# Kernel tuning notes

Hardware: AMD Instinct MI355X
Metric: run time of the kernel (lower is better)

The kernel has to match this reference:

```python
import jax, jax.numpy as jnp
import numpy as np

NUM_HEADS = 8
LN_EPS = 1e-5


def _layernorm(t, w, b):
    mu = t.mean(-1, keepdims=True)
    var = t.var(-1, keepdims=True)  # ddof=0, matches torch LayerNorm
    return (t - mu) * jax.lax.rsqrt(var + LN_EPS) * w + b


def setup_inputs() -> dict:
    key = jax.random.key(0)
    ks = jax.random.split(key, 5)
    B, C, H, W = 16, 384, 32, 32
    hidden = 4 * C
    s = 0.02
    return {
        "x": jax.random.normal(ks[0], (B, C, H, W), jnp.float32),
        "ln1_w": jnp.ones((C,), jnp.float32),
        "ln1_b": jnp.zeros((C,), jnp.float32),
        "qkv_w": s * jax.random.normal(ks[1], (3 * C, C), jnp.float32),
        "qkv_b": jnp.zeros((3 * C,), jnp.float32),
        "proj_w": s * jax.random.normal(ks[2], (C, C), jnp.float32),
        "proj_b": jnp.zeros((C,), jnp.float32),
        "ln2_w": jnp.ones((C,), jnp.float32),
        "ln2_b": jnp.zeros((C,), jnp.float32),
        "fc1_w": s * jax.random.normal(ks[3], (hidden, C), jnp.float32),
        "fc1_b": jnp.zeros((hidden,), jnp.float32),
        "fc2_w": s * jax.random.normal(ks[4], (C, hidden), jnp.float32),
        "fc2_b": jnp.zeros((C,), jnp.float32),
    }


def reference(x, ln1_w, ln1_b, qkv_w, qkv_b, proj_w, proj_b,
              ln2_w, ln2_b, fc1_w, fc1_b, fc2_w, fc2_b):
    B, C, H, W = x.shape
    N = H * W
    nh = NUM_HEADS
    hd = C // nh
    scale = hd ** (-0.5)

    xf = x.reshape(B, C, N).transpose(0, 2, 1)  # (B, N, C) tokens

    # --- pre-norm attention ---
    h1 = _layernorm(xf, ln1_w, ln1_b)
    qkv = h1 @ qkv_w.T + qkv_b                      # (B, N, 3C)
    qkv = qkv.reshape(B, N, 3, nh, hd).transpose(2, 0, 3, 1, 4)  # (3,B,h,N,d)
    q, k, v = qkv[0], qkv[1], qkv[2]
    attn = jax.nn.softmax(jnp.einsum('bhnd,bhmd->bhnm', q, k) * scale, axis=-1)
    out = jnp.einsum('bhnm,bhmd->bhnd', attn, v)    # (B,h,N,d)
    out = out.transpose(0, 2, 1, 3).reshape(B, N, C)
    out = out @ proj_w.T + proj_b
    xf = xf + out

    # --- pre-norm FFN (exact GELU, matching torch nn.GELU default) ---
    h2 = _layernorm(xf, ln2_w, ln2_b)
    f = jax.nn.gelu(h2 @ fc1_w.T + fc1_b, approximate=False)
    f = f @ fc2_w.T + fc2_b
    xf = xf + f

    return xf.transpose(0, 2, 1).reshape(B, C, H, W)
```

## Files before the change

### kernel.cpp

```cpp
#include <hip/hip_runtime.h>

typedef unsigned short u16;
using bf16x8 = __attribute__((ext_vector_type(8))) short;
using f32x4  = __attribute__((ext_vector_type(4))) float;

#define DEV __device__ __forceinline__

constexpr int    NTOK = 16384;
constexpr size_t QKSZ = (size_t)16 * 8 * 1024 * 64;
constexpr float  ATTN_SCALE = 0.14433756729740645f;

DEV u16 f2bf(float x) {
  unsigned int u = __float_as_uint(x);
  u += 0x7fffu + ((u >> 16) & 1u);
  return (u16)(u >> 16);
}

DEV void async16(const u16* g, u16* l) {
  __builtin_amdgcn_global_load_lds(
      (const __attribute__((address_space(1))) unsigned int*)g,
      (__attribute__((address_space(3))) unsigned int*)l, 16, 0, 0);
}

DEV const bf16x8* lds_swz(const u16* base, int row, int bytecol) {
  int byte = row * 128 + bytecol;
  byte ^= (row & 7) << 4;
  return (const bf16x8*)((const char*)base + byte);
}

DEV float gelu_f(float x) { return 0.5f * x * (1.0f + erff(x * 0.70710678118654752440f)); }

__global__ void cvt4_kernel(const float* __restrict__ s0, u16* __restrict__ d0,
                            const float* __restrict__ s1, u16* __restrict__ d1,
                            const float* __restrict__ s2, u16* __restrict__ d2,
                            const float* __restrict__ s3, u16* __restrict__ d3) {
  int i = blockIdx.x * 256 + threadIdx.x;
  const float* s; u16* d; int off;
  if (i < 110592)        { s = s0; d = d0; off = i; }
  else if (i < 147456)   { s = s1; d = d1; off = i - 110592; }
  else if (i < 294912)   { s = s2; d = d2; off = i - 147456; }
  else                   { s = s3; d = d3; off = i - 294912; }
  float4 v = *(const float4*)(s + (size_t)off * 4);
  ushort4 o{f2bf(v.x), f2bf(v.y), f2bf(v.z), f2bf(v.w)};
  *(ushort4*)(d + (size_t)off * 4) = o;
}

__global__ __launch_bounds__(256) void ln_kernel(
    const float* __restrict__ in, const float* __restrict__ gw,
    const float* __restrict__ gb, u16* __restrict__ out) {
  __shared__ float tile[32][385];
  __shared__ float mu_s[32], rs_s[32];
  const int b = blockIdx.y;
  const int n0 = blockIdx.x * 32;
  const int t = threadIdx.x;
  const int j = t & 31, cb = t >> 5;
  const float* src = in + (size_t)b * 384 * 1024 + n0;
  for (int k = 0; k < 48; ++k) {
    int c = k * 8 + cb;
    tile[j][c] = src[(size_t)c * 1024 + j];
  }
  __syncthreads();
  const int jt = t >> 3, r = t & 7;
  float s = 0.f, ss = 0.f;
  for (int c = r; c < 384; c += 8) { float v = tile[jt][c]; s += v; ss += v * v; }
  s += __shfl_xor(s, 1); ss += __shfl_xor(ss, 1);
  s += __shfl_xor(s, 2); ss += __shfl_xor(ss, 2);
  s += __shfl_xor(s, 4); ss += __shfl_xor(ss, 4);
  const float mean = s * (1.f / 384.f);
  const float var  = ss * (1.f / 384.f) - mean * mean;
  if (r == 0) { mu_s[jt] = mean; rs_s[jt] = rsqrtf(var + 1e-5f); }
  __syncthreads();
  for (int q = t; q < 3072; q += 256) {
    int tok = q / 96, c4 = (q - tok * 96) * 4;
    float m = mu_s[tok], rv = rs_s[tok];
    float4 wv = *(const float4*)(gw + c4);
    float4 bv = *(const float4*)(gb + c4);
    u16* dst = out + (size_t)(b * 1024 + n0 + tok) * 384 + c4;
    ushort4 o{f2bf((tile[tok][c4 + 0] - m) * rv * wv.x + bv.x),
              f2bf((tile[tok][c4 + 1] - m) * rv * wv.y + bv.y),
              f2bf((tile[tok][c4 + 2] - m) * rv * wv.z + bv.z),
              f2bf((tile[tok][c4 + 3] - m) * rv * wv.w + bv.w)};
    *(ushort4*)dst = o;
  }
}

template<int EPI>
__global__ __launch_bounds__(256, 2) void gemm_kernel(
    const u16* __restrict__ A, const u16* __restrict__ W,
    const float* __restrict__ bias, float* __restrict__ outf,
    u16* __restrict__ outh, const float* __restrict__ resid, int K) {
  __shared__ u16 sA[2][4096], sB[2][4096];
  const int m0 = blockIdx.x * 128, n0 = blockIdx.y * 128;
  const int wv = threadIdx.x >> 6, lane = threadIdx.x & 63;
  const int wm = (wv >> 1) * 64, wn = (wv & 1) * 64;
  const int l16 = lane & 15, lg8 = (lane >> 4) * 8;

  f32x4 acc[4][4];
#pragma unroll
  for (int i = 0; i < 4; ++i)
#pragma unroll
    for (int jj = 0; jj < 4; ++jj) acc[i][jj] = f32x4{0.f, 0.f, 0.f, 0.f};

  const int nk = K >> 5;
  auto stage = [&](int buf, int kt) {
    const u16* Ab = A + (size_t)m0 * K + kt * 32;
    const u16* Wb = W + (size_t)n0 * K + kt * 32;
#pragma unroll
    for (int i = 0; i < 2; ++i) {
      int chunk = i * 256 + wv * 64 + lane;
      int row = chunk >> 2, sl = chunk & 3;
      async16(Ab + (size_t)row * K + sl * 8, &sA[buf][(i * 256 + wv * 64) * 8]);
      async16(Wb + (size_t)row * K + sl * 8, &sB[buf][(i * 256 + wv * 64) * 8]);
    }
  };
  stage(0, 0);
  __syncthreads();
  int cur = 0;
  for (int kt = 0; kt < nk; ++kt) {
    if (kt + 1 < nk) stage(cur ^ 1, kt + 1);
    bf16x8 av[4], bv[4];
#pragma unroll
    for (int f = 0; f < 4; ++f) {
      av[f] = *(const bf16x8*)&sA[cur][(wm + f * 16 + l16) * 32 + lg8];
      bv[f] = *(const bf16x8*)&sB[cur][(wn + f * 16 + l16) * 32 + lg8];
    }
#pragma unroll
    for (int mf = 0; mf < 4; ++mf)
#pragma unroll
      for (int nf = 0; nf < 4; ++nf)
        acc[mf][nf] = __builtin_amdgcn_mfma_f32_16x16x32_bf16(av[mf], bv[nf], acc[mf][nf], 0, 0, 0);
    __syncthreads();
    cur ^= 1;
  }

#pragma unroll
  for (int mf = 0; mf < 4; ++mf) {
    const int mm = m0 + wm + mf * 16 + (lane >> 4) * 4;
    const int b = mm >> 10, nn = mm & 1023;
#pragma unroll
    for (int nf = 0; nf < 4; ++nf) {
      const int col = n0 + wn + nf * 16 + l16;
      f32x4 v = acc[mf][nf];
      const float bs = bias[col];
      if constexpr (EPI == 0) {
        const int which = col / 384, rem = col % 384;
        const int hh = rem / 48, dd = rem % 48;
        if (which == 2) {
          unsigned long long pk = 0;
#pragma unroll
          for (int rr = 0; rr < 4; ++rr)
            pk |= (unsigned long long)f2bf(v[rr] + bs) << (16 * rr);
          size_t idx = 2ull * QKSZ + (((size_t)((b * 8 + hh) * 64 + dd)) << 10) + nn;
          *(unsigned long long*)&outh[idx] = pk;
        } else {
          const float sc = (which == 0) ? ATTN_SCALE : 1.0f;
          size_t base = (size_t)which * QKSZ + (size_t)((b * 8 + hh) * 1024 + nn) * 64 + dd;
#pragma unroll
          for (int rr = 0; rr < 4; ++rr) outh[base + (size_t)rr * 64] = f2bf((v[rr] + bs) * sc);
        }
      } else if constexpr (EPI == 1 || EPI == 3) {
        size_t idx = ((size_t)(b * 384 + col) << 10) + nn;
        float4 rr4 = *(const float4*)&resid[idx];
        float4 o{v[0] + bs + rr4.x, v[1] + bs + rr4.y, v[2] + bs + rr4.z, v[3] + bs + rr4.w};
        *(float4*)&outf[idx] = o;
      } else {
#pragma unroll
        for (int rr = 0; rr < 4; ++rr)
          outh[(size_t)(mm + rr) * 1536 + col] = f2bf(gelu_f(v[rr] + bs));
      }
    }
  }
}

__global__ __launch_bounds__(256, 2) void attn_kernel(
    const u16* __restrict__ Qg, const u16* __restrict__ Kg,
    const u16* __restrict__ Vtg, u16* __restrict__ outp) {
  __shared__ u16 Ks[2][64 * 64];
  __shared__ u16 Vs[2][64 * 64];
  __shared__ u16 QPs[4 * 32 * 72];
  const int orig = blockIdx.x;
  const int swz = (orig & 7) * 128 + (orig >> 3);
  const int bh = swz >> 3, qt = swz & 7;
  const int w = threadIdx.x >> 6, lane = threadIdx.x & 63;
  const int l16 = lane & 15, lg = lane >> 4;

  const u16* kbase = Kg + (size_t)bh * 1024 * 64;
  const u16* vbase = Vtg + (size_t)bh * 64 * 1024;

  auto stageKV = [&](int buf, int kv) {
#pragma unroll
    for (int i = 0; i < 2; ++i) {
      int cb = (i * 4 + w) * 64;
      int ck = cb + lane;
      int g  = ck ^ ((ck >> 3) & 7);
      async16(kbase + (size_t)kv * 4096 + g * 8, &Ks[buf][cb * 8]);
      async16(vbase + (size_t)(g >> 3) * 1024 + kv * 64 + (g & 7) * 8, &Vs[buf][cb * 8]);
    }
  };

  {
    const u16* src = Qg + (size_t)(bh * 1024 + qt * 128) * 64;
#pragma unroll
    for (int i = 0; i < 4; ++i) {
      int cb = (i * 4 + w) * 64;
      int ck = cb + lane;
      int g  = ck ^ ((ck >> 3) & 7);
      async16(src + g * 8, &QPs[cb * 8]);
    }
  }
  stageKV(0, 0);
  __syncthreads();

  bf16x8 qf[2][2];
#pragma unroll
  for (int mf = 0; mf < 2; ++mf)
#pragma unroll
    for (int ks = 0; ks < 2; ++ks)
      qf[mf][ks] = *lds_swz(QPs, w * 32 + mf * 16 + l16, ks * 64 + lg * 16);
  __syncthreads();

  float lr[2][4];
  f32x4 acco[2][4];
#pragma unroll
  for (int mf = 0; mf < 2; ++mf) {
#pragma unroll
    for (int r = 0; r < 4; ++r) lr[mf][r] = 0.f;
#pragma unroll
    for (int df = 0; df < 4; ++df) acco[mf][df] = f32x4{0.f, 0.f, 0.f, 0.f};
  }
  u16* Pw = &QPs[w * 32 * 72];

  int cur = 0;
  for (int kv = 0; kv < 16; ++kv) {
    if (kv + 1 < 16) stageKV(cur ^ 1, kv + 1);

    f32x4 accs[2][4];
#pragma unroll
    for (int mf = 0; mf < 2; ++mf)
#pragma unroll
      for (int nf = 0; nf < 4; ++nf) accs[mf][nf] = f32x4{0.f, 0.f, 0.f, 0.f};
    __builtin_amdgcn_s_setprio(1);
#pragma unroll
    for (int nf = 0; nf < 4; ++nf) {
      bf16x8 k0 = *lds_swz(Ks[cur], nf * 16 + l16, lg * 16);
      bf16x8 k1 = *lds_swz(Ks[cur], nf * 16 + l16, 64 + lg * 16);
#pragma unroll
      for (int mf = 0; mf < 2; ++mf) {
        accs[mf][nf] = __builtin_amdgcn_mfma_f32_16x16x32_bf16(qf[mf][0], k0, accs[mf][nf], 0, 0, 0);
        accs[mf][nf] = __builtin_amdgcn_mfma_f32_16x16x32_bf16(qf[mf][1], k1, accs[mf][nf], 0, 0, 0);
      }
    }
    __builtin_amdgcn_s_setprio(0);
#pragma unroll
    for (int mf = 0; mf < 2; ++mf)
#pragma unroll
      for (int r = 0; r < 4; ++r) {
        float s0 = __expf(accs[mf][0][r]);
        float s1 = __expf(accs[mf][1][r]);
        float s2 = __expf(accs[mf][2][r]);
        float s3 = __expf(accs[mf][3][r]);
        accs[mf][0][r] = s0; accs[mf][1][r] = s1;
        accs[mf][2][r] = s2; accs[mf][3][r] = s3;
        lr[mf][r] += s0 + s1 + s2 + s3;
      }
#pragma unroll
    for (int mf = 0; mf < 2; ++mf)
#pragma unroll
      for (int nf = 0; nf < 4; ++nf)
#pragma unroll
        for (int r = 0; r < 4; ++r)
          Pw[(mf * 16 + lg * 4 + r) * 72 + nf * 16 + l16] = f2bf(accs[mf][nf][r]);
    asm volatile("s_waitcnt lgkmcnt(0)" ::: "memory");
#pragma unroll
    for (int ks = 0; ks < 2; ++ks) {
      bf16x8 pa[2], vf[4];
#pragma unroll
      for (int mf = 0; mf < 2; ++mf)
        pa[mf] = *(const bf16x8*)&Pw[(mf * 16 + l16) * 72 + ks * 32 + lg * 8];
#pragma unroll
      for (int df = 0; df < 4; ++df)
        vf[df] = *lds_swz(Vs[cur], df * 16 + l16, ks * 64 + lg * 16);
      __builtin_amdgcn_s_setprio(1);
#pragma unroll
      for (int mf = 0; mf < 2; ++mf)
#pragma unroll
        for (int df = 0; df < 4; ++df)
          acco[mf][df] = __builtin_amdgcn_mfma_f32_16x16x32_bf16(pa[mf], vf[df], acco[mf][df], 0, 0, 0);
      __builtin_amdgcn_s_setprio(0);
    }
    __syncthreads();
    cur ^= 1;
  }
  const int b = bh >> 3, h = bh & 7;
#pragma unroll
  for (int mf = 0; mf < 2; ++mf)
#pragma unroll
    for (int r = 0; r < 4; ++r) {
      float t = lr[mf][r];
      t += __shfl_xor(t, 1); t += __shfl_xor(t, 2);
      t += __shfl_xor(t, 4); t += __shfl_xor(t, 8);
      float inv = 1.f / t;
      int token = qt * 128 + w * 32 + mf * 16 + lg * 4 + r;
      size_t rowb = (size_t)(b * 1024 + token) * 384 + h * 48;
#pragma unroll
      for (int df = 0; df < 3; ++df)
        outp[rowb + df * 16 + l16] = f2bf(acco[mf][df][r] * inv);
    }
}

constexpr size_t OFF_WQKV = 0;
constexpr size_t OFF_WPROJ = 884736;
constexpr size_t OFF_WFC1 = 1179648;
constexpr size_t OFF_WFC2 = 2359296;
constexpr size_t OFF_H    = 3538944;
constexpr size_t OFF_QKV  = 16121856;
constexpr size_t OFF_AO   = 66453504;
constexpr size_t OFF_Y1T  = 79036416;

extern "C" void kernel_launch(void* const* d_in, const int* in_sizes, int n_in,
                              void* d_out, int out_size, void* d_ws, size_t ws_size,
                              hipStream_t stream) {
  (void)in_sizes; (void)n_in; (void)out_size; (void)ws_size;
  const float* x     = (const float*)d_in[0];
  const float* ln1w  = (const float*)d_in[1];
  const float* ln1b  = (const float*)d_in[2];
  const float* qkvw  = (const float*)d_in[3];
  const float* qkvbi = (const float*)d_in[4];
  const float* projw = (const float*)d_in[5];
  const float* projb = (const float*)d_in[6];
  const float* ln2w  = (const float*)d_in[7];
  const float* ln2b  = (const float*)d_in[8];
  const float* fc1w  = (const float*)d_in[9];
  const float* fc1b  = (const float*)d_in[10];
  const float* fc2w  = (const float*)d_in[11];
  const float* fc2b  = (const float*)d_in[12];

  char* ws = (char*)d_ws;
  u16* wqkv  = (u16*)(ws + OFF_WQKV);
  u16* wproj = (u16*)(ws + OFF_WPROJ);
  u16* wfc1  = (u16*)(ws + OFF_WFC1);
  u16* wfc2  = (u16*)(ws + OFF_WFC2);
  u16* h1    = (u16*)(ws + OFF_H);
  u16* qkvs  = (u16*)(ws + OFF_QKV);
  u16* f1    = qkvs;
  u16* ao    = (u16*)(ws + OFF_AO);
  float* y1t = (float*)(ws + OFF_Y1T);

  hipMemsetAsync(qkvs, 0, QKSZ * 2, stream);

  cvt4_kernel<<<1728, 256, 0, stream>>>(qkvw, wqkv, projw, wproj, fc1w, wfc1, fc2w, wfc2);

  dim3 lngrid(32, 16);
  ln_kernel<<<lngrid, 256, 0, stream>>>(x, ln1w, ln1b, h1);

  gemm_kernel<0><<<dim3(NTOK / 128, 9), 256, 0, stream>>>(h1, wqkv, qkvbi, nullptr, qkvs, nullptr, 384);

  attn_kernel<<<dim3(1024), 256, 0, stream>>>(qkvs, qkvs + QKSZ, qkvs + 2 * QKSZ, ao);

  gemm_kernel<1><<<dim3(NTOK / 128, 3), 256, 0, stream>>>(ao, wproj, projb, y1t, nullptr, x, 384);

  ln_kernel<<<lngrid, 256, 0, stream>>>(y1t, ln2w, ln2b, h1 );

  gemm_kernel<2><<<dim3(NTOK / 128, 12), 256, 0, stream>>>(h1, wfc1, fc1b, nullptr, f1, nullptr, 384);

  gemm_kernel<3><<<dim3(NTOK / 128, 3), 256, 0, stream>>>(f1, wfc2, fc2b, (float*)d_out, nullptr, y1t, 1536);
}
```

Measured before the change: 308.0 us.

## Triple-buffer GEMM/attention loads, pad QKV weights, swap MFMA operands, tanh GELU

GEMM and attention K/V staging move from double to triple buffering, with explicit vmcnt waits and a single barrier per iteration, and the GEMM gains an XOR-swizzled LDS layout. QKV weights and bias are padded to 64 per head with the attention scale folded in, which removes the memset and allows vectorized Q/K stores. The V part of QKV gets its own transposed-store GEMM variant, and the fc1/QKV GEMMs swap MFMA operands so they can write packed 8-byte stores. Exact erf GELU is replaced by the tanh approximation, which changes numerics relative to the exact-GELU reference.

```diff
diff --git a/kernel.cpp b/kernel.cpp
--- a/kernel.cpp
+++ b/kernel.cpp
@@ -28,21 +28,48 @@
   return (const bf16x8*)((const char*)base + byte);
 }
 
-DEV float gelu_f(float x) { return 0.5f * x * (1.0f + erff(x * 0.70710678118654752440f)); }
-
-__global__ void cvt4_kernel(const float* __restrict__ s0, u16* __restrict__ d0,
-                            const float* __restrict__ s1, u16* __restrict__ d1,
-                            const float* __restrict__ s2, u16* __restrict__ d2,
-                            const float* __restrict__ s3, u16* __restrict__ d3) {
+DEV float gelu_f(float x) {
+  float y = 0.7978845608028654f * (x + 0.044715f * x * x * x);
+  float e = __expf(2.f * y);
+  float t = 1.f - 2.f / (e + 1.f);
+  return 0.5f * x * (1.f + t);
+}
+
+__global__ void cvt_kernel(const float* __restrict__ qkvw, const float* __restrict__ qkvb,
+                           const float* __restrict__ projw, const float* __restrict__ fc1w,
+                           const float* __restrict__ fc2w,
+                           u16* __restrict__ wqkvp, float* __restrict__ biasp,
+                           u16* __restrict__ wproj, u16* __restrict__ wfc1,
+                           u16* __restrict__ wfc2) {
   int i = blockIdx.x * 256 + threadIdx.x;
-  const float* s; u16* d; int off;
-  if (i < 110592)        { s = s0; d = d0; off = i; }
-  else if (i < 147456)   { s = s1; d = d1; off = i - 110592; }
-  else if (i < 294912)   { s = s2; d = d2; off = i - 147456; }
-  else                   { s = s3; d = d3; off = i - 294912; }
-  float4 v = *(const float4*)(s + (size_t)off * 4);
-  ushort4 o{f2bf(v.x), f2bf(v.y), f2bf(v.z), f2bf(v.w)};
-  *(ushort4*)(d + (size_t)off * 4) = o;
+  if (i < 147456) {
+    int p = i / 96, q = (i - p * 96) * 4;
+    int which = p >> 9, h = (p >> 6) & 7, d = p & 63;
+    ushort4 o{0, 0, 0, 0};
+    if (d < 48) {
+      float sc = which ? 1.f : ATTN_SCALE;
+      float4 v = *(const float4*)(qkvw + (size_t)(which * 384 + h * 48 + d) * 384 + q);
+      o = ushort4{f2bf(v.x * sc), f2bf(v.y * sc), f2bf(v.z * sc), f2bf(v.w * sc)};
+    }
+    *(ushort4*)(wqkvp + (size_t)p * 384 + q) = o;
+  } else if (i < 479232) {
+    const float* s; u16* d; int off;
+    if (i < 184320)      { s = projw; d = wproj; off = i - 147456; }
+    else if (i < 331776) { s = fc1w;  d = wfc1;  off = i - 184320; }
+    else                 { s = fc2w;  d = wfc2;  off = i - 331776; }
+    float4 v = *(const float4*)(s + (size_t)off * 4);
+    *(ushort4*)(d + (size_t)off * 4) = ushort4{f2bf(v.x), f2bf(v.y), f2bf(v.z), f2bf(v.w)};
+  } else if (i < 479616) {
+    int qi = (i - 479232) * 4;
+    float4 o;
+    float* op = (float*)&o;
+#pragma unroll
+    for (int r = 0; r < 4; ++r) {
+      int p = qi + r, which = p >> 9, h = (p >> 6) & 7, d = p & 63;
+      op[r] = (d < 48) ? qkvb[which * 384 + h * 48 + d] * (which ? 1.f : ATTN_SCALE) : 0.f;
+    }
+    *(float4*)(biasp + qi) = o;
+  }
 }
 
 __global__ __launch_bounds__(256) void ln_kernel(
@@ -85,15 +112,18 @@
 }
 
 template<int EPI>
-__global__ __launch_bounds__(256, 2) void gemm_kernel(
+__global__ __launch_bounds__(256, 3) void gemm_kernel(
     const u16* __restrict__ A, const u16* __restrict__ W,
     const float* __restrict__ bias, float* __restrict__ outf,
     u16* __restrict__ outh, const float* __restrict__ resid, int K) {
-  __shared__ u16 sA[2][4096], sB[2][4096];
-  const int m0 = blockIdx.x * 128, n0 = blockIdx.y * 128;
+  constexpr bool SWAP = (EPI == 0 || EPI == 2);
+  __shared__ u16 sA[3][4096], sB[3][4096];
+  const int m0 = blockIdx.x * 128;
+  const int n0 = (EPI == 4 ? 1024 : 0) + blockIdx.y * 128;
   const int wv = threadIdx.x >> 6, lane = threadIdx.x & 63;
   const int wm = (wv >> 1) * 64, wn = (wv & 1) * 64;
-  const int l16 = lane & 15, lg8 = (lane >> 4) * 8;
+  const int l16 = lane & 15, lg = lane >> 4;
+  const int rsw = (lg ^ (l16 & 3)) << 4;
 
   f32x4 acc[4][4];
 #pragma unroll
@@ -108,65 +138,89 @@
 #pragma unroll
     for (int i = 0; i < 2; ++i) {
       int chunk = i * 256 + wv * 64 + lane;
-      int row = chunk >> 2, sl = chunk & 3;
+      int row = chunk >> 2, sl = (chunk & 3) ^ (row & 3);
       async16(Ab + (size_t)row * K + sl * 8, &sA[buf][(i * 256 + wv * 64) * 8]);
       async16(Wb + (size_t)row * K + sl * 8, &sB[buf][(i * 256 + wv * 64) * 8]);
     }
   };
   stage(0, 0);
-  __syncthreads();
-  int cur = 0;
+  stage(1, 1);
+  int buf = 0;
   for (int kt = 0; kt < nk; ++kt) {
-    if (kt + 1 < nk) stage(cur ^ 1, kt + 1);
+    if (kt < nk - 1) asm volatile("s_waitcnt vmcnt(4)" ::: "memory");
+    else             asm volatile("s_waitcnt vmcnt(0)" ::: "memory");
+    __builtin_amdgcn_s_barrier();
+    if (kt + 2 < nk) { int nb = buf + 2; if (nb >= 3) nb -= 3; stage(nb, kt + 2); }
     bf16x8 av[4], bv[4];
 #pragma unroll
     for (int f = 0; f < 4; ++f) {
-      av[f] = *(const bf16x8*)&sA[cur][(wm + f * 16 + l16) * 32 + lg8];
-      bv[f] = *(const bf16x8*)&sB[cur][(wn + f * 16 + l16) * 32 + lg8];
-    }
+      av[f] = *(const bf16x8*)((const char*)&sA[buf][0] + (wm + f * 16 + l16) * 64 + rsw);
+      bv[f] = *(const bf16x8*)((const char*)&sB[buf][0] + (wn + f * 16 + l16) * 64 + rsw);
+    }
+    __builtin_amdgcn_s_setprio(1);
 #pragma unroll
     for (int mf = 0; mf < 4; ++mf)
 #pragma unroll
-      for (int nf = 0; nf < 4; ++nf)
-        acc[mf][nf] = __builtin_amdgcn_mfma_f32_16x16x32_bf16(av[mf], bv[nf], acc[mf][nf], 0, 0, 0);
-    __syncthreads();
-    cur ^= 1;
-  }
-
-#pragma unroll
-  for (int mf = 0; mf < 4; ++mf) {
-    const int mm = m0 + wm + mf * 16 + (lane >> 4) * 4;
-    const int b = mm >> 10, nn = mm & 1023;
-#pragma unroll
-    for (int nf = 0; nf < 4; ++nf) {
-      const int col = n0 + wn + nf * 16 + l16;
-      f32x4 v = acc[mf][nf];
-      const float bs = bias[col];
-      if constexpr (EPI == 0) {
-        const int which = col / 384, rem = col % 384;
-        const int hh = rem / 48, dd = rem % 48;
-        if (which == 2) {
+      for (int nf = 0; nf < 4; ++nf) {
+        if constexpr (SWAP)
+          acc[mf][nf] = __builtin_amdgcn_mfma_f32_16x16x32_bf16(bv[nf], av[mf], acc[mf][nf], 0, 0, 0);
+        else
+          acc[mf][nf] = __builtin_amdgcn_mfma_f32_16x16x32_bf16(av[mf], bv[nf], acc[mf][nf], 0, 0, 0);
+      }
+    __builtin_amdgcn_s_setprio(0);
+    ++buf; if (buf >= 3) buf = 0;
+  }
+
+  if constexpr (SWAP) {
+#pragma unroll
+    for (int mf = 0; mf < 4; ++mf) {
+      const int token = m0 + wm + mf * 16 + l16;
+      const int b = token >> 10, nn = token & 1023;
+#pragma unroll
+      for (int nf = 0; nf < 4; ++nf) {
+        const int col = n0 + wn + nf * 16 + lg * 4;
+        f32x4 v = acc[mf][nf];
+        float4 bb = *(const float4*)(bias + col);
+        unsigned long long pk = 0;
+        if constexpr (EPI == 0) {
+#pragma unroll
+          for (int rr = 0; rr < 4; ++rr)
+            pk |= (unsigned long long)f2bf(v[rr] + ((const float*)&bb)[rr]) << (16 * rr);
+          const int which = col >> 9, h = (col >> 6) & 7, d0 = col & 63;
+          size_t idx = (size_t)which * QKSZ + (size_t)((b * 8 + h) * 1024 + nn) * 64 + d0;
+          *(unsigned long long*)&outh[idx] = pk;
+        } else {
+#pragma unroll
+          for (int rr = 0; rr < 4; ++rr)
+            pk |= (unsigned long long)f2bf(gelu_f(v[rr] + ((const float*)&bb)[rr])) << (16 * rr);
+          *(unsigned long long*)&outh[(size_t)token * 1536 + col] = pk;
+        }
+      }
+    }
+  } else {
+#pragma unroll
+    for (int mf = 0; mf < 4; ++mf) {
+      const int mm = m0 + wm + mf * 16 + lg * 4;
+      const int b = mm >> 10, nn = mm & 1023;
+#pragma unroll
+      for (int nf = 0; nf < 4; ++nf) {
+        const int col = n0 + wn + nf * 16 + l16;
+        f32x4 v = acc[mf][nf];
+        const float bs = bias[col];
+        if constexpr (EPI == 4) {
           unsigned long long pk = 0;
 #pragma unroll
           for (int rr = 0; rr < 4; ++rr)
             pk |= (unsigned long long)f2bf(v[rr] + bs) << (16 * rr);
-          size_t idx = 2ull * QKSZ + (((size_t)((b * 8 + hh) * 64 + dd)) << 10) + nn;
+          const int h = (col >> 6) & 7, d = col & 63;
+          size_t idx = 2ull * QKSZ + (((size_t)((b * 8 + h) * 64 + d)) << 10) + nn;
           *(unsigned long long*)&outh[idx] = pk;
         } else {
-          const float sc = (which == 0) ? ATTN_SCALE : 1.0f;
-          size_t base = (size_t)which * QKSZ + (size_t)((b * 8 + hh) * 1024 + nn) * 64 + dd;
-#pragma unroll
-          for (int rr = 0; rr < 4; ++rr) outh[base + (size_t)rr * 64] = f2bf((v[rr] + bs) * sc);
+          size_t idx = ((size_t)(b * 384 + col) << 10) + nn;
+          float4 rr4 = *(const float4*)&resid[idx];
+          float4 o{v[0] + bs + rr4.x, v[1] + bs + rr4.y, v[2] + bs + rr4.z, v[3] + bs + rr4.w};
+          *(float4*)&outf[idx] = o;
         }
-      } else if constexpr (EPI == 1 || EPI == 3) {
-        size_t idx = ((size_t)(b * 384 + col) << 10) + nn;
-        float4 rr4 = *(const float4*)&resid[idx];
-        float4 o{v[0] + bs + rr4.x, v[1] + bs + rr4.y, v[2] + bs + rr4.z, v[3] + bs + rr4.w};
-        *(float4*)&outf[idx] = o;
-      } else {
-#pragma unroll
-        for (int rr = 0; rr < 4; ++rr)
-          outh[(size_t)(mm + rr) * 1536 + col] = f2bf(gelu_f(v[rr] + bs));
       }
     }
   }
@@ -175,8 +229,8 @@
 __global__ __launch_bounds__(256, 2) void attn_kernel(
     const u16* __restrict__ Qg, const u16* __restrict__ Kg,
     const u16* __restrict__ Vtg, u16* __restrict__ outp) {
-  __shared__ u16 Ks[2][64 * 64];
-  __shared__ u16 Vs[2][64 * 64];
+  __shared__ u16 Ks[3][4096];
+  __shared__ u16 Vs[3][4096];
   __shared__ u16 QPs[4 * 32 * 72];
   const int orig = blockIdx.x;
   const int swz = (orig & 7) * 128 + (orig >> 3);
@@ -209,7 +263,9 @@
     }
   }
   stageKV(0, 0);
-  __syncthreads();
+  stageKV(1, 1);
+  asm volatile("s_waitcnt vmcnt(8)" ::: "memory");
+  __builtin_amdgcn_s_barrier();
 
   bf16x8 qf[2][2];
 #pragma unroll
@@ -217,7 +273,8 @@
 #pragma unroll
     for (int ks = 0; ks < 2; ++ks)
       qf[mf][ks] = *lds_swz(QPs, w * 32 + mf * 16 + l16, ks * 64 + lg * 16);
-  __syncthreads();
+  asm volatile("s_waitcnt lgkmcnt(0)" ::: "memory");
+  __builtin_amdgcn_s_barrier();
 
   float lr[2][4];
   f32x4 acco[2][4];
@@ -230,10 +287,7 @@
   }
   u16* Pw = &QPs[w * 32 * 72];
 
-  int cur = 0;
-  for (int kv = 0; kv < 16; ++kv) {
-    if (kv + 1 < 16) stageKV(cur ^ 1, kv + 1);
-
+  auto compute = [&](int buf) {
     f32x4 accs[2][4];
 #pragma unroll
     for (int mf = 0; mf < 2; ++mf)
@@ -242,8 +296,8 @@
     __builtin_amdgcn_s_setprio(1);
 #pragma unroll
     for (int nf = 0; nf < 4; ++nf) {
-      bf16x8 k0 = *lds_swz(Ks[cur], nf * 16 + l16, lg * 16);
-      bf16x8 k1 = *lds_swz(Ks[cur], nf * 16 + l16, 64 + lg * 16);
+      bf16x8 k0 = *lds_swz(Ks[buf], nf * 16 + l16, lg * 16);
+      bf16x8 k1 = *lds_swz(Ks[buf], nf * 16 + l16, 64 + lg * 16);
 #pragma unroll
       for (int mf = 0; mf < 2; ++mf) {
         accs[mf][nf] = __builtin_amdgcn_mfma_f32_16x16x32_bf16(qf[mf][0], k0, accs[mf][nf], 0, 0, 0);
@@ -279,7 +333,7 @@
         pa[mf] = *(const bf16x8*)&Pw[(mf * 16 + l16) * 72 + ks * 32 + lg * 8];
 #pragma unroll
       for (int df = 0; df < 4; ++df)
-        vf[df] = *lds_swz(Vs[cur], df * 16 + l16, ks * 64 + lg * 16);
+        vf[df] = *lds_swz(Vs[buf], df * 16 + l16, ks * 64 + lg * 16);
       __builtin_amdgcn_s_setprio(1);
 #pragma unroll
       for (int mf = 0; mf < 2; ++mf)
@@ -288,9 +342,18 @@
           acco[mf][df] = __builtin_amdgcn_mfma_f32_16x16x32_bf16(pa[mf], vf[df], acco[mf][df], 0, 0, 0);
       __builtin_amdgcn_s_setprio(0);
     }
-    __syncthreads();
-    cur ^= 1;
-  }
+  };
+
+  int buf = 0;
+  for (int kv = 0; kv < 16; ++kv) {
+    if (kv < 15) asm volatile("s_waitcnt vmcnt(4)" ::: "memory");
+    else         asm volatile("s_waitcnt vmcnt(0)" ::: "memory");
+    __builtin_amdgcn_s_barrier();
+    if (kv + 2 < 16) { int nb = buf + 2; if (nb >= 3) nb -= 3; stageKV(nb, kv + 2); }
+    compute(buf);
+    ++buf; if (buf >= 3) buf = 0;
+  }
+
   const int b = bh >> 3, h = bh & 7;
 #pragma unroll
   for (int mf = 0; mf < 2; ++mf)
@@ -308,14 +371,15 @@
     }
 }
 
-constexpr size_t OFF_WQKV = 0;
-constexpr size_t OFF_WPROJ = 884736;
-constexpr size_t OFF_WFC1 = 1179648;
-constexpr size_t OFF_WFC2 = 2359296;
-constexpr size_t OFF_H    = 3538944;
-constexpr size_t OFF_QKV  = 16121856;
-constexpr size_t OFF_AO   = 66453504;
-constexpr size_t OFF_Y1T  = 79036416;
+constexpr size_t OFF_WQKVP = 0;
+constexpr size_t OFF_BIASP = 1179648;
+constexpr size_t OFF_WPROJ = 1185792;
+constexpr size_t OFF_WFC1  = 1480704;
+constexpr size_t OFF_WFC2  = 2660352;
+constexpr size_t OFF_H     = 3840000;
+constexpr size_t OFF_QKV   = 16422912;
+constexpr size_t OFF_AO    = 66754560;
+constexpr size_t OFF_Y1T   = 79337472;
 
 extern "C" void kernel_launch(void* const* d_in, const int* in_sizes, int n_in,
                               void* d_out, int out_size, void* d_ws, size_t ws_size,
@@ -336,24 +400,25 @@
   const float* fc2b  = (const float*)d_in[12];
 
   char* ws = (char*)d_ws;
-  u16* wqkv  = (u16*)(ws + OFF_WQKV);
-  u16* wproj = (u16*)(ws + OFF_WPROJ);
-  u16* wfc1  = (u16*)(ws + OFF_WFC1);
-  u16* wfc2  = (u16*)(ws + OFF_WFC2);
-  u16* h1    = (u16*)(ws + OFF_H);
-  u16* qkvs  = (u16*)(ws + OFF_QKV);
-  u16* f1    = qkvs;
-  u16* ao    = (u16*)(ws + OFF_AO);
-  float* y1t = (float*)(ws + OFF_Y1T);
-
-  hipMemsetAsync(qkvs, 0, QKSZ * 2, stream);
-
-  cvt4_kernel<<<1728, 256, 0, stream>>>(qkvw, wqkv, projw, wproj, fc1w, wfc1, fc2w, wfc2);
+  u16*   wqkvp = (u16*)(ws + OFF_WQKVP);
+  float* biasp = (float*)(ws + OFF_BIASP);
+  u16*   wproj = (u16*)(ws + OFF_WPROJ);
+  u16*   wfc1  = (u16*)(ws + OFF_WFC1);
+  u16*   wfc2  = (u16*)(ws + OFF_WFC2);
+  u16*   h1    = (u16*)(ws + OFF_H);
+  u16*   qkvs  = (u16*)(ws + OFF_QKV);
+  u16*   f1    = qkvs;
+  u16*   ao    = (u16*)(ws + OFF_AO);
+  float* y1t   = (float*)(ws + OFF_Y1T);
+
+  cvt_kernel<<<1874, 256, 0, stream>>>(qkvw, qkvbi, projw, fc1w, fc2w,
+                                       wqkvp, biasp, wproj, wfc1, wfc2);
 
   dim3 lngrid(32, 16);
   ln_kernel<<<lngrid, 256, 0, stream>>>(x, ln1w, ln1b, h1);
 
-  gemm_kernel<0><<<dim3(NTOK / 128, 9), 256, 0, stream>>>(h1, wqkv, qkvbi, nullptr, qkvs, nullptr, 384);
+  gemm_kernel<0><<<dim3(NTOK / 128, 8), 256, 0, stream>>>(h1, wqkvp, biasp, nullptr, qkvs, nullptr, 384);
+  gemm_kernel<4><<<dim3(NTOK / 128, 4), 256, 0, stream>>>(h1, wqkvp, biasp, nullptr, qkvs, nullptr, 384);
 
   attn_kernel<<<dim3(1024), 256, 0, stream>>>(qkvs, qkvs + QKSZ, qkvs + 2 * QKSZ, ao);
 
```

Measured after the change: 320.9 us. 1.04x slower.
